# Performance work log

Measured on AMD Instinct MI355X. Metric: run time of the kernel, lower is better.

The kernel has to match this reference:

```python
import jax, jax.numpy as jnp
import numpy as np

B, N, E = 8, 4096, 65536
FIN, OUT, T, H = 128, 128, 4, 4
C = OUT // H  # per-head channels
NEG_SLOPE = 0.2
EPS_LN = 1e-5


def setup_inputs() -> dict:
    key = jax.random.key(0)
    ks = jax.random.split(key, 10)
    x = jax.random.normal(ks[0], (B, N, FIN), dtype=jnp.float32)
    edge_index = jax.random.randint(ks[1], (B, 2, E), 0, N, dtype=jnp.int64)
    edge_type = jax.random.randint(ks[2], (B, E), 0, T, dtype=jnp.int64)
    # per-edge-type GATConv params (PyG GATConv: lin weight, att_src, att_dst, bias)
    W = jax.random.normal(ks[3], (T, FIN, H * C), dtype=jnp.float32) / np.sqrt(FIN)
    a_src = jax.random.normal(ks[4], (T, H, C), dtype=jnp.float32) / np.sqrt(C)
    a_dst = jax.random.normal(ks[5], (T, H, C), dtype=jnp.float32) / np.sqrt(C)
    bias = jnp.zeros((T, H * C), dtype=jnp.float32)
    gamma = jnp.ones((OUT,), dtype=jnp.float32)
    beta = jnp.zeros((OUT,), dtype=jnp.float32)
    return {"x": x, "edge_index": edge_index, "edge_type": edge_type,
            "W": W, "a_src": a_src, "a_dst": a_dst, "bias": bias,
            "gamma": gamma, "beta": beta}


def _gat_aggregate(h, src, dst, mask):
    """Single-graph masked GAT aggregation.
    h: [N,H,C] transformed features; src,dst: [E]; mask: [E] bool.
    Returns [N,H,C].
    """
    n = h.shape[0]
    a_s = h[src]                     # [E,H,C] source features (messages)
    # attention logits: att_src . h_src + att_dst . h_dst, done by caller via h-dot
    return a_s, n


def reference(x, edge_index, edge_type, W, a_src, a_dst, bias, gamma, beta):
    b, n, _ = x.shape
    src = edge_index[:, 0, :]  # [B,E]
    dst = edge_index[:, 1, :]

    def per_graph(e_logit, src_b, dst_b, mask_b, h_b):
        # e_logit: [E,H]; h_b: [N,H,C]
        e_m = jnp.where(mask_b[:, None], e_logit, -1e30)
        m = jax.ops.segment_max(e_m, dst_b, num_segments=n)      # [N,H]
        m = jnp.maximum(m, -1e30)
        ex = jnp.exp(e_m - m[dst_b]) * mask_b[:, None]           # [E,H]
        den = jax.ops.segment_sum(ex, dst_b, num_segments=n)     # [N,H]
        alpha = ex / (den[dst_b] + 1e-16)                        # [E,H]
        msg = alpha[:, :, None] * h_b[src_b]                     # [E,H,C]
        return jax.ops.segment_sum(msg, dst_b, num_segments=n)   # [N,H,C]

    out = jnp.zeros((b, n, H * C), dtype=x.dtype)
    for t in range(T):
        h = jnp.einsum('bnf,fo->bno', x, W[t]).reshape(b, n, H, C)
        al_s = jnp.einsum('bnhc,hc->bnh', h, a_src[t])           # [B,N,H]
        al_d = jnp.einsum('bnhc,hc->bnh', h, a_dst[t])
        e = jax.nn.leaky_relu(
            jnp.take_along_axis(al_s, src[..., None], axis=1) +
            jnp.take_along_axis(al_d, dst[..., None], axis=1),
            negative_slope=NEG_SLOPE)                            # [B,E,H]
        mask = (edge_type == t)
        agg = jax.vmap(per_graph)(e, src, dst, mask, h)          # [B,N,H,C]
        out = out + agg.reshape(b, n, H * C) + bias[t]
    # residual + LayerNorm (dropout is identity in eval)
    y = x + out
    mu = jnp.mean(y, axis=-1, keepdims=True)
    var = jnp.var(y, axis=-1, keepdims=True)
    return (y - mu) / jnp.sqrt(var + EPS_LN) * gamma + beta
```

## Files before the change

kernel.cpp:

```cpp
#include <hip/hip_runtime.h>

typedef unsigned int uint;
typedef unsigned short ushort;
typedef __attribute__((ext_vector_type(8))) short short8;
typedef __attribute__((ext_vector_type(4))) float f32x4;

#define Bb 8
#define Nn 4096
#define Ee 65536
#define Tt 4

__device__ __forceinline__ ushort bf16_rne_u(float f) {
    uint u = __float_as_uint(f);
    u += 0x7FFFu + ((u >> 16) & 1u);
    return (ushort)(u >> 16);
}

__global__ __launch_bounds__(256) void fused_a_kernel(
    const int* __restrict__ ei, const int* __restrict__ et, uint* __restrict__ count,
    const float* __restrict__ W, ushort* __restrict__ Wf,
    const float* __restrict__ bias, float* __restrict__ bias_sum)
{
    int bid = blockIdx.x;
    int tid = threadIdx.x;
    if (bid < 2048) {
        int i = bid * 256 + tid;
        int b = i >> 16;
        int e = i & (Ee - 1);
        int dst = ei[(size_t)b * 2 * Ee + Ee + e];
        int t = et[(size_t)b * Ee + e];
        atomicAdd(&count[(((uint)(b * Nn + dst)) << 2) | (uint)t], 1u);
    } else if (bid < 2080) {
        int gid = (bid - 2048) * 256 + tid;
        int t    = gid >> 11;
        int rem  = gid & 2047;
        int ks   = rem >> 9;
        int rem2 = rem & 511;
        int nt   = rem2 >> 6;
        int lane = rem2 & 63;
        int n  = nt * 16 + (lane & 15);
        int g  = lane >> 4;
        int k0 = ks * 32 + 4 * g;
        const float* Wt = W + t * 16384;
        union { uint4 q; ushort u[8]; } P;
#pragma unroll
        for (int j = 0; j < 4; ++j) P.u[j]     = bf16_rne_u(Wt[(size_t)(k0 + j) * 128 + n]);
#pragma unroll
        for (int j = 0; j < 4; ++j) P.u[4 + j] = bf16_rne_u(Wt[(size_t)(k0 + 16 + j) * 128 + n]);
        *reinterpret_cast<uint4*>(Wf + (size_t)gid * 8) = P.q;
    } else {
        if (tid < 128)
            bias_sum[tid] = bias[tid] + bias[128 + tid] + bias[256 + tid] + bias[384 + tid];
    }
}

__global__ __launch_bounds__(256, 4) void fused_b_kernel(
    const float* __restrict__ x, const ushort* __restrict__ Wf,
    const float* __restrict__ a_src, const float* __restrict__ a_dst,
    ushort* __restrict__ h, float* __restrict__ al_s, float* __restrict__ al_d,
    const uint* __restrict__ cnt, uint* __restrict__ offs, uint* __restrict__ bsum)
{
    __shared__ ushort Wlds[16384];
    __shared__ ushort Hst[4096];

    int tid = threadIdx.x;

    if (blockIdx.x >= 1024) {
        uint* ws = reinterpret_cast<uint*>(Hst);
        int cblk = blockIdx.x - 1024;
        int lane = tid & 63, wv = tid >> 6;
        uint4 c = reinterpret_cast<const uint4*>(cnt)[cblk * 256 + tid];
        uint tot = c.x + c.y + c.z + c.w;
        uint inc = tot;
#pragma unroll
        for (int d = 1; d < 64; d <<= 1) {
            uint tv = (uint)__shfl_up((int)inc, d);
            if (lane >= d) inc += tv;
        }
        if (lane == 63) ws[wv] = inc;
        __syncthreads();
        uint wexcl = 0;
        for (int w = 0; w < wv; ++w) wexcl += ws[w];
        uint P = wexcl + inc - tot;
        uint4 o;
        o.x = P; o.y = P + c.x; o.z = o.y + c.y; o.w = o.z + c.z;
        reinterpret_cast<uint4*>(offs)[cblk * 256 + tid] = o;
        if (tid == 255) bsum[cblk] = P + tot;
        return;
    }

    int blk    = blockIdx.x;
    int b      = blk >> 7;
    int rowblk = blk & 127;
    int w    = tid >> 6;
    int lane = tid & 63;
    int nl = lane & 15;
    int g  = lane >> 4;
    int rg  = w & 1;
    int chn = w >> 1;
    int row0 = rowblk * 32 + rg * 16;

    short8 Ah[4], Al[4];
    {
        const float* xr = x + ((size_t)b * Nn + row0 + nl) * 128;
#pragma unroll
        for (int ks = 0; ks < 4; ++ks) {
            float4 fa = *reinterpret_cast<const float4*>(xr + ks * 32 + 4 * g);
            float4 fb = *reinterpret_cast<const float4*>(xr + ks * 32 + 16 + 4 * g);
            float v[8] = {fa.x, fa.y, fa.z, fa.w, fb.x, fb.y, fb.z, fb.w};
            union { short8 s; ushort u[8]; } H, L;
#pragma unroll
            for (int j = 0; j < 8; ++j) {
                ushort hi = bf16_rne_u(v[j]);
                float fh = __uint_as_float(((uint)hi) << 16);
                H.u[j] = hi;
                L.u[j] = bf16_rne_u(v[j] - fh);
            }
            Ah[ks] = H.s;
            Al[ks] = L.s;
        }
    }

    for (int t = 0; t < Tt; ++t) {
        {
            const uint4* src = reinterpret_cast<const uint4*>(Wf + (size_t)t * 16384);
#pragma unroll
            for (int i = 0; i < 8; ++i) {
                uint4 v = src[i * 256 + tid];
                *reinterpret_cast<uint4*>(&Wlds[(i * 256 + tid) * 8]) = v;
            }
        }
        __syncthreads();

        f32x4 acc[4];
#pragma unroll
        for (int i = 0; i < 4; ++i) acc[i] = (f32x4){0.f, 0.f, 0.f, 0.f};
#pragma unroll
        for (int ks = 0; ks < 4; ++ks) {
#pragma unroll
            for (int i = 0; i < 4; ++i) {
                int ntg = chn * 4 + i;
                union { uint4 q; short8 s; } F;
                F.q = *reinterpret_cast<const uint4*>(&Wlds[((ks * 8 + ntg) * 64 + lane) * 8]);
                acc[i] = __builtin_amdgcn_mfma_f32_16x16x32_bf16(Ah[ks], F.s, acc[i], 0, 0, 0);
                acc[i] = __builtin_amdgcn_mfma_f32_16x16x32_bf16(Al[ks], F.s, acc[i], 0, 0, 0);
            }
        }

        {
            float as[4], ad[4];
#pragma unroll
            for (int i = 0; i < 4; ++i) {
                as[i] = a_src[t * 128 + chn * 64 + i * 16 + nl];
                ad[i] = a_dst[t * 128 + chn * 64 + i * 16 + nl];
            }
#pragma unroll
            for (int ih = 0; ih < 2; ++ih) {
#pragma unroll
                for (int r = 0; r < 4; ++r) {
                    float ps = acc[2 * ih][r] * as[2 * ih] + acc[2 * ih + 1][r] * as[2 * ih + 1];
                    float pd = acc[2 * ih][r] * ad[2 * ih] + acc[2 * ih + 1][r] * ad[2 * ih + 1];
#pragma unroll
                    for (int off = 1; off < 16; off <<= 1) {
                        ps += __shfl_xor(ps, off);
                        pd += __shfl_xor(pd, off);
                    }
                    if (nl == 0) {
                        int rowg = row0 + 4 * g + r;
                        int head = 2 * chn + ih;
                        al_s[((size_t)(b * Tt + t) * Nn + rowg) * 4 + head] = ps;
                        al_d[((size_t)(b * Tt + t) * Nn + rowg) * 4 + head] = pd;
                    }
                }
            }
        }

#pragma unroll
        for (int i = 0; i < 4; ++i) {
#pragma unroll
            for (int r = 0; r < 4; ++r) {
                int rowl = rg * 16 + 4 * g + r;
                int col  = chn * 64 + i * 16 + nl;
                uint e = (uint)(rowl * 128) + ((uint)col ^ (uint)(((rowl >> 2) & 3) << 3));
                Hst[e] = bf16_rne_u(acc[i][r]);
            }
        }
        __syncthreads();

        {
            ushort* hb = h + ((size_t)(b * Tt + t) * Nn + (size_t)rowblk * 32) * 128;
#pragma unroll
            for (int it = 0; it < 2; ++it) {
                uint f = (uint)(it * 2048 + tid * 8);
                int rowl = f >> 7;
                uint e = (f & ~127u) + ((f & 127u) ^ (uint)(((rowl >> 2) & 3) << 3));
                uint4 v = *reinterpret_cast<const uint4*>(&Hst[e]);
                *reinterpret_cast<uint4*>(hb + f) = v;
            }
        }
    }
}

__global__ __launch_bounds__(128) void scan2_kernel(
    const uint* __restrict__ bsum, uint* __restrict__ bsx)
{
    __shared__ uint w0tot;
    int tid = threadIdx.x, lane = tid & 63, wv = tid >> 6;
    uint v = bsum[tid], inc = v;
#pragma unroll
    for (int d = 1; d < 64; d <<= 1) {
        uint tv = (uint)__shfl_up((int)inc, d);
        if (lane >= d) inc += tv;
    }
    if (tid == 63) w0tot = inc;
    __syncthreads();
    uint add = (wv == 1) ? w0tot : 0u;
    bsx[tid] = add + inc - v;
}

__global__ __launch_bounds__(256) void scatter_lr_kernel(
    const int* __restrict__ ei, const int* __restrict__ et,
    const float* __restrict__ al_s, const float* __restrict__ al_d,
    const uint* __restrict__ offs, const uint* __restrict__ bsx,
    uint* __restrict__ cursor, uint* __restrict__ src_sorted, float4* __restrict__ lr_sorted)
{
    int i = blockIdx.x * 256 + threadIdx.x;
    int b = i >> 16;
    int e = i & (Ee - 1);
    int src = ei[(size_t)b * 2 * Ee + e];
    int dst = ei[(size_t)b * 2 * Ee + Ee + e];
    int t = et[(size_t)b * Ee + e];
    uint g = (((uint)(b * Nn + dst)) << 2) | (uint)t;
    uint slot = atomicAdd(&cursor[g], 1u);
    uint p = offs[g] + bsx[g >> 10] + slot;

    size_t btN = (size_t)(b * Tt + t) * Nn;
    float4 s4 = *reinterpret_cast<const float4*>(&al_s[(btN + src) * 4]);
    float4 d4 = *reinterpret_cast<const float4*>(&al_d[(btN + dst) * 4]);
    float4 lr;
    lr.x = s4.x + d4.x; lr.x = lr.x > 0.f ? lr.x : 0.2f * lr.x;
    lr.y = s4.y + d4.y; lr.y = lr.y > 0.f ? lr.y : 0.2f * lr.y;
    lr.z = s4.z + d4.z; lr.z = lr.z > 0.f ? lr.z : 0.2f * lr.z;
    lr.w = s4.w + d4.w; lr.w = lr.w > 0.f ? lr.w : 0.2f * lr.w;
    src_sorted[p] = (uint)src;
    lr_sorted[p] = lr;
}

__global__ __launch_bounds__(256) void gat_ln_kernel(
    const float* __restrict__ x, const ushort* __restrict__ h,
    const uint* __restrict__ count, const uint* __restrict__ offs, const uint* __restrict__ bsx,
    const uint* __restrict__ src_sorted, const float4* __restrict__ lr_sorted,
    const float* __restrict__ bias_sum, const float* __restrict__ gamma, const float* __restrict__ beta,
    float* __restrict__ out)
{
    __shared__ uint  su_s[16][96];
    __shared__ float ew_s[16][96 * 4];

    int tid = threadIdx.x;
    int wl   = tid >> 6;
    int lane = tid & 63;
    int ng = lane >> 4;
    int cl = lane & 15;
    int c0 = cl << 3;
    int hh = cl >> 2;
    int grp = wl * 4 + ng;
    uint*  su = su_s[grp];
    float* ew = ew_s[grp];

    int wid = blockIdx.x * 16 + grp;
    int b   = wid >> 12;
    int dst = wid & (Nn - 1);

    uint4 cnt4 = reinterpret_cast<const uint4*>(count)[wid];
    uint4 off4 = reinterpret_cast<const uint4*>(offs)[wid];
    uint base  = off4.x + bsx[((uint)wid) >> 8];
    uint D     = min(off4.w + cnt4.w - off4.x, 96u);

    for (uint i = cl; i < D; i += 16) {
        float4 l4 = lr_sorted[base + i];
        su[i] = src_sorted[base + i];
        ew[i * 4 + 0] = __expf(l4.x);
        ew[i * 4 + 1] = __expf(l4.y);
        ew[i * 4 + 2] = __expf(l4.z);
        ew[i * 4 + 3] = __expf(l4.w);
    }
    __syncthreads();

    uint rel[4] = {0u, off4.y - off4.x, off4.z - off4.x, off4.w - off4.x};
    uint ctv[4] = {cnt4.x, cnt4.y, cnt4.z, cnt4.w};

    float tot[8];
#pragma unroll
    for (int k = 0; k < 8; ++k) tot[k] = 0.f;

#pragma unroll
    for (int t = 0; t < Tt; ++t) {
        uint ct = ctv[t];
        if (!ct) continue;
        uint p0 = rel[t];
        const ushort* hs = h + (size_t)(b * Tt + t) * Nn * 128;

        float acc[8];
#pragma unroll
        for (int k = 0; k < 8; ++k) acc[k] = 0.f;
        float den = 0.f;

        for (uint j = 0; j < ct; ++j) {
            uint i = p0 + j;
            float aw = ew[i * 4 + hh];
            uint  sj = su[i];
            uint4 hv = *reinterpret_cast<const uint4*>(hs + (size_t)sj * 128 + c0);
            float f0 = __uint_as_float(hv.x << 16);
            float f1 = __uint_as_float(hv.x & 0xFFFF0000u);
            float f2 = __uint_as_float(hv.y << 16);
            float f3 = __uint_as_float(hv.y & 0xFFFF0000u);
            float f4 = __uint_as_float(hv.z << 16);
            float f5 = __uint_as_float(hv.z & 0xFFFF0000u);
            float f6 = __uint_as_float(hv.w << 16);
            float f7 = __uint_as_float(hv.w & 0xFFFF0000u);
            acc[0] += aw * f0; acc[1] += aw * f1;
            acc[2] += aw * f2; acc[3] += aw * f3;
            acc[4] += aw * f4; acc[5] += aw * f5;
            acc[6] += aw * f6; acc[7] += aw * f7;
            den += aw;
        }
        float rden = 1.f / (den + 1e-16f);
#pragma unroll
        for (int k = 0; k < 8; ++k) tot[k] += acc[k] * rden;
    }

    size_t obase = ((size_t)b * Nn + dst) * 128 + c0;
    float y[8];
    {
        float4 xa = *reinterpret_cast<const float4*>(x + obase);
        float4 xb = *reinterpret_cast<const float4*>(x + obase + 4);
        float4 ba = *reinterpret_cast<const float4*>(bias_sum + c0);
        float4 bb = *reinterpret_cast<const float4*>(bias_sum + c0 + 4);
        y[0] = xa.x + tot[0] + ba.x; y[1] = xa.y + tot[1] + ba.y;
        y[2] = xa.z + tot[2] + ba.z; y[3] = xa.w + tot[3] + ba.w;
        y[4] = xb.x + tot[4] + bb.x; y[5] = xb.y + tot[5] + bb.y;
        y[6] = xb.z + tot[6] + bb.z; y[7] = xb.w + tot[7] + bb.w;
    }

    float s = 0.f, ss = 0.f;
#pragma unroll
    for (int k = 0; k < 8; ++k) { s += y[k]; ss += y[k] * y[k]; }
#pragma unroll
    for (int off = 1; off < 16; off <<= 1) {
        s += __shfl_xor(s, off);
        ss += __shfl_xor(ss, off);
    }
    float mu = s * (1.f / 128.f);
    float var = ss * (1.f / 128.f) - mu * mu;
    float rstd = rsqrtf(var + 1e-5f);

    float4 ga = *reinterpret_cast<const float4*>(gamma + c0);
    float4 gb = *reinterpret_cast<const float4*>(gamma + c0 + 4);
    float4 ea = *reinterpret_cast<const float4*>(beta + c0);
    float4 eb = *reinterpret_cast<const float4*>(beta + c0 + 4);
    float4 o1, o2;
    o1.x = (y[0] - mu) * rstd * ga.x + ea.x;
    o1.y = (y[1] - mu) * rstd * ga.y + ea.y;
    o1.z = (y[2] - mu) * rstd * ga.z + ea.z;
    o1.w = (y[3] - mu) * rstd * ga.w + ea.w;
    o2.x = (y[4] - mu) * rstd * gb.x + eb.x;
    o2.y = (y[5] - mu) * rstd * gb.y + eb.y;
    o2.z = (y[6] - mu) * rstd * gb.z + eb.z;
    o2.w = (y[7] - mu) * rstd * gb.w + eb.w;
    *reinterpret_cast<float4*>(out + obase) = o1;
    *reinterpret_cast<float4*>(out + obase + 4) = o2;
}

extern "C" void kernel_launch(void* const* d_in, const int* in_sizes, int n_in,
                              void* d_out, int out_size, void* d_ws, size_t ws_size,
                              hipStream_t stream)
{
    const float* x     = (const float*)d_in[0];
    const int*   ei    = (const int*)d_in[1];
    const int*   et    = (const int*)d_in[2];
    const float* W     = (const float*)d_in[3];
    const float* a_src = (const float*)d_in[4];
    const float* a_dst = (const float*)d_in[5];
    const float* bias  = (const float*)d_in[6];
    const float* gamma = (const float*)d_in[7];
    const float* beta  = (const float*)d_in[8];
    float* out = (float*)d_out;

    ushort* h   = (ushort*)d_ws;
    size_t hsz  = (size_t)Bb * Tt * Nn * 128;
    float* al_s = (float*)(h + hsz);
    size_t alsz = (size_t)Bb * Tt * Nn * 4;
    float* al_d = al_s + alsz;
    uint* count  = (uint*)(al_d + alsz);
    uint* cursor = count + (size_t)Bb * Tt * Nn;
    uint* offs   = cursor + (size_t)Bb * Tt * Nn;
    uint* bsum   = offs + (size_t)Bb * Tt * Nn;
    uint* bsx    = bsum + 128;
    float* bias_sum = (float*)(bsx + 128);
    uint* src_sorted = (uint*)(bias_sum + 128);
    float4* lr_sorted = (float4*)(src_sorted + (size_t)Bb * Ee);
    ushort* Wf = (ushort*)(lr_sorted + (size_t)Bb * Ee);

    hipMemsetAsync(count, 0, (size_t)Bb * Tt * Nn * 2 * sizeof(uint), stream);

    fused_a_kernel<<<2081, 256, 0, stream>>>(ei, et, count, W, Wf, bias, bias_sum);
    fused_b_kernel<<<1152, 256, 0, stream>>>(x, Wf, a_src, a_dst, h, al_s, al_d,
                                             count, offs, bsum);
    scan2_kernel<<<1, 128, 0, stream>>>(bsum, bsx);
    scatter_lr_kernel<<<(Bb * Ee) / 256, 256, 0, stream>>>(
        ei, et, al_s, al_d, offs, bsx, cursor, src_sorted, lr_sorted);
    gat_ln_kernel<<<(Bb * Nn) / 16, 256, 0, stream>>>(
        x, h, count, offs, bsx, src_sorted, lr_sorted, bias_sum, gamma, beta, out);
}
```

Measured before the change: 186.3 us.

## Load MFMA weight fragments directly from global and use per-wave output staging

Drops the shared-memory staging of the per-type weight matrix and has each wave load its bf16 B-fragments straight from global memory (L2-resident, reused across blocks). The output tile is staged in a per-wave swizzled LDS buffer, so both block-wide __syncthreads per edge type go away and LDS use shrinks from about 40KB to 8KB, which could allow more resident blocks. In exchange, each wave issues more global loads for the weights, with no cross-wave reuse, and the per-wave LDS round trip relies on intra-wave ordering with no barrier.

```diff
diff --git a/kernel.cpp b/kernel.cpp
--- a/kernel.cpp
+++ b/kernel.cpp
@@ -60,13 +60,12 @@
     ushort* __restrict__ h, float* __restrict__ al_s, float* __restrict__ al_d,
     const uint* __restrict__ cnt, uint* __restrict__ offs, uint* __restrict__ bsum)
 {
-    __shared__ ushort Wlds[16384];
-    __shared__ ushort Hst[4096];
+    __shared__ ushort Hst[4][1024];
 
     int tid = threadIdx.x;
 
     if (blockIdx.x >= 1024) {
-        uint* ws = reinterpret_cast<uint*>(Hst);
+        uint* ws = reinterpret_cast<uint*>(&Hst[0][0]);
         int cblk = blockIdx.x - 1024;
         int lane = tid & 63, wv = tid >> 6;
         uint4 c = reinterpret_cast<const uint4*>(cnt)[cblk * 256 + tid];
@@ -99,6 +98,7 @@
     int rg  = w & 1;
     int chn = w >> 1;
     int row0 = rowblk * 32 + rg * 16;
+    ushort* hw = Hst[w];
 
     short8 Ah[4], Al[4];
     {
@@ -121,29 +121,22 @@
         }
     }
 
+    const uint4* Wfq = reinterpret_cast<const uint4*>(Wf);
+
     for (int t = 0; t < Tt; ++t) {
-        {
-            const uint4* src = reinterpret_cast<const uint4*>(Wf + (size_t)t * 16384);
-#pragma unroll
-            for (int i = 0; i < 8; ++i) {
-                uint4 v = src[i * 256 + tid];
-                *reinterpret_cast<uint4*>(&Wlds[(i * 256 + tid) * 8]) = v;
-            }
-        }
-        __syncthreads();
-
         f32x4 acc[4];
 #pragma unroll
         for (int i = 0; i < 4; ++i) acc[i] = (f32x4){0.f, 0.f, 0.f, 0.f};
 #pragma unroll
         for (int ks = 0; ks < 4; ++ks) {
+            union { uint4 q; short8 s; } F[4];
+#pragma unroll
+            for (int i = 0; i < 4; ++i)
+                F[i].q = Wfq[(((t * 4 + ks) * 8) + chn * 4 + i) * 64 + lane];
 #pragma unroll
             for (int i = 0; i < 4; ++i) {
-                int ntg = chn * 4 + i;
-                union { uint4 q; short8 s; } F;
-                F.q = *reinterpret_cast<const uint4*>(&Wlds[((ks * 8 + ntg) * 64 + lane) * 8]);
-                acc[i] = __builtin_amdgcn_mfma_f32_16x16x32_bf16(Ah[ks], F.s, acc[i], 0, 0, 0);
-                acc[i] = __builtin_amdgcn_mfma_f32_16x16x32_bf16(Al[ks], F.s, acc[i], 0, 0, 0);
+                acc[i] = __builtin_amdgcn_mfma_f32_16x16x32_bf16(Ah[ks], F[i].s, acc[i], 0, 0, 0);
+                acc[i] = __builtin_amdgcn_mfma_f32_16x16x32_bf16(Al[ks], F[i].s, acc[i], 0, 0, 0);
             }
         }
 
@@ -179,23 +172,21 @@
         for (int i = 0; i < 4; ++i) {
 #pragma unroll
             for (int r = 0; r < 4; ++r) {
-                int rowl = rg * 16 + 4 * g + r;
-                int col  = chn * 64 + i * 16 + nl;
-                uint e = (uint)(rowl * 128) + ((uint)col ^ (uint)(((rowl >> 2) & 3) << 3));
-                Hst[e] = bf16_rne_u(acc[i][r]);
-            }
-        }
-        __syncthreads();
+                int rowl  = 4 * g + r;
+                int colws = i * 16 + nl;
+                hw[rowl * 64 + (colws ^ ((rowl & 3) << 3))] = bf16_rne_u(acc[i][r]);
+            }
+        }
 
         {
-            ushort* hb = h + ((size_t)(b * Tt + t) * Nn + (size_t)rowblk * 32) * 128;
-#pragma unroll
-            for (int it = 0; it < 2; ++it) {
-                uint f = (uint)(it * 2048 + tid * 8);
-                int rowl = f >> 7;
-                uint e = (f & ~127u) + ((f & 127u) ^ (uint)(((rowl >> 2) & 3) << 3));
-                uint4 v = *reinterpret_cast<const uint4*>(&Hst[e]);
-                *reinterpret_cast<uint4*>(hb + f) = v;
+            ushort* hb = h + ((size_t)(b * Tt + t) * Nn + row0) * 128 + chn * 64;
+#pragma unroll
+            for (int p = 0; p < 2; ++p) {
+                int task = p * 64 + lane;
+                int rowl = task >> 3;
+                int c8   = (task & 7) * 8;
+                uint4 v = *reinterpret_cast<const uint4*>(&hw[rowl * 64 + (c8 ^ ((rowl & 3) << 3))]);
+                *reinterpret_cast<uint4*>(hb + (size_t)rowl * 128 + c8) = v;
             }
         }
     }
```

Result: faster. 181.6 us (-2.5%).
